# Optimization experiments

Measured on AMD Instinct MI355X. Metric: run time of the kernel, lower is better.

Reference implementation:

```python
import jax, jax.numpy as jnp
import numpy as np
import math

N = 30000        # nodes
E = 390000       # edges (first N are self-loops, in node order)
H = 64
NNS = 4          # num_node_states
NES = 4          # num_edge_states
NGRAPH = 64      # graphs in batch
TEMP_ON_EVAL = 1.0


def from_binary(bits):
    # bits: [..., k] of {0,1} -> integer code sum(bits * 2^k)
    pw = (2 ** jnp.arange(bits.shape[-1])).astype(bits.dtype)
    return jnp.sum(bits * pw, axis=-1)


def segment_softmax(logits, seg, num_seg, tau):
    m = jax.ops.segment_max(logits, seg, num_segments=num_seg)
    e = jnp.exp((logits - m[seg]) / tau)
    s = jax.ops.segment_sum(e, seg, num_segments=num_seg)
    return e / s[seg]


def segment_hard_onehot(logits, seg, num_seg):
    # gumbel_softmax with tau=0, no noise: one-hot at per-segment argmax (first on ties)
    n = logits.shape[0]
    m = jax.ops.segment_max(logits, seg, num_segments=num_seg)
    idx = jnp.where(logits >= m[seg], jnp.arange(n, dtype=jnp.int32), jnp.int32(n))
    first = jax.ops.segment_min(idx, seg, num_segments=num_seg)
    return (jnp.arange(n, dtype=jnp.int32) == first[seg]).astype(jnp.int32)


def select_best(emb, bits, scalars, index, num_index):
    # SelectBest with use_select_best=True. states are even ints < 2^(k+1);
    # unique((states, index)) groups == fused key states*num_index+index.
    states = 2 * from_binary(bits)
    key = states * num_index + index
    num_key = (2 ** (bits.shape[-1] + 1)) * num_index
    best = segment_hard_onehot(-scalars[:, 0], key, num_key)
    return emb[states + best]


def temp_by_step(step, upper, lower, num_iter, temp_on_eval):
    if step == -1:
        return temp_on_eval
    frac = min(float(step) / num_iter, 1.0)
    return upper + (lower - upper) * frac


def forward(node_states, edge_states, scalars, edge_index, batch_vec, rev_idx,
            emb_edge, emb_sbv, emb_sbr, emb_static,
            Wq, Wk, Wv, Wek, Wev, Wc, training_step):
    ei0, ei1 = edge_index[0], edge_index[1]
    # self-loop edges are the first N edges in node order ->
    # scalars[edge_index[0]==edge_index[1]] == scalars[:N]
    node_scalars = scalars[:N]                                   # [N,1]

    # select_best_from_virtual
    node_fts = select_best(emb_sbv, node_states, node_scalars, batch_vec, NGRAPH)  # [N,H]
    edge_fts = emb_edge[from_binary(edge_states)]                # [E,H]

    Q = node_fts @ Wq.T
    K = node_fts @ Wk.T
    V = node_fts @ Wv.T

    # combined_edge_KV
    sb = select_best(emb_sbr, node_states[ei0], scalars, ei1, N)  # [E,H]
    edge_K = sb @ Wek.T
    sender_s = node_scalars[ei0]                                  # [E,1]
    reciever_s = node_scalars[ei1]                                # [E,1]
    rlx = (scalars < reciever_s)
    rlx_d = (sender_s + scalars < reciever_s)
    fts = jnp.concatenate([rlx, rlx_d], axis=-1).astype(jnp.int32)  # [E,2] bits
    static_fts = emb_static[from_binary(fts)]                     # [E,H]
    combined = jnp.concatenate([edge_fts, edge_fts[rev_idx], static_fts], axis=1)  # [E,3H]
    edge_V = combined @ Wc.T                                      # [E,H]

    # compute_message
    Qe = Q[ei1]
    Ke = K[ei0] + edge_K
    Ve = V[ei0] + edge_V
    alpha = jnp.sum(Qe * Ke, axis=-1) / math.sqrt(H)              # [E]
    tau = temp_by_step(int(training_step), 3.0, 0.1, 10000, TEMP_ON_EVAL)
    alpha = segment_softmax(alpha, ei1, N, tau)
    message = Ve * alpha[:, None]                                  # [E,H]

    node_out = node_fts + jax.ops.segment_sum(message, ei1, num_segments=N)
    edge_out = edge_fts + message
    return node_out, edge_out


def setup_inputs() -> dict:
    key = jax.random.key(0)
    ks = jax.random.split(key, 16)
    node_states = jax.random.randint(ks[0], (N, NNS), 0, 2, dtype=jnp.int32)
    edge_states = jax.random.randint(ks[1], (E, NES), 0, 2, dtype=jnp.int32)
    scalars = jax.random.normal(ks[2], (E, 1), dtype=jnp.float32)
    loops = jnp.arange(N, dtype=jnp.int32)
    senders = jax.random.randint(ks[3], (E - N,), 0, N, dtype=jnp.int32)
    receivers = jax.random.randint(ks[4], (E - N,), 0, N, dtype=jnp.int32)
    edge_index = jnp.stack([jnp.concatenate([loops, senders]),
                            jnp.concatenate([loops, receivers])])  # [2,E]
    batch_vec = jnp.sort(jax.random.randint(ks[5], (N,), 0, NGRAPH, dtype=jnp.int32))
    rev_idx = jax.random.permutation(ks[6], E).astype(jnp.int32)
    s = 0.05
    return {
        'node_states': node_states, 'edge_states': edge_states, 'scalars': scalars,
        'edge_index': edge_index, 'batch_vec': batch_vec, 'rev_idx': rev_idx,
        'emb_edge': s * jax.random.normal(ks[7], (2 ** NES, H), dtype=jnp.float32),
        'emb_sbv': s * jax.random.normal(ks[8], (2 ** (NNS + 1), H), dtype=jnp.float32),
        'emb_sbr': s * jax.random.normal(ks[9], (2 ** (NNS + 1), H), dtype=jnp.float32),
        'emb_static': s * jax.random.normal(ks[10], (4, H), dtype=jnp.float32),
        'Wq': s * jax.random.normal(ks[11], (H, H), dtype=jnp.float32),
        'Wk': s * jax.random.normal(ks[12], (H, H), dtype=jnp.float32),
        'Wv': s * jax.random.normal(ks[13], (H, H), dtype=jnp.float32),
        'Wek': s * jax.random.normal(ks[14], (H, H), dtype=jnp.float32),
        'Wev': s * jax.random.normal(ks[15], (H, H), dtype=jnp.float32),
        'Wc': s * jax.random.normal(jax.random.fold_in(key, 99), (H, 3 * H), dtype=jnp.float32),
        'training_step': -1,
    }


def reference(node_states, edge_states, scalars, edge_index, batch_vec, rev_idx,
              emb_edge, emb_sbv, emb_sbr, emb_static,
              Wq, Wk, Wv, Wek, Wev, Wc, training_step):
    return forward(node_states, edge_states, scalars, edge_index, batch_vec, rev_idx,
                   emb_edge, emb_sbv, emb_sbr, emb_static,
                   Wq, Wk, Wv, Wek, Wev, Wc, training_step)
```

## Files before the change

kernel.cpp:

```cpp
#include <hip/hip_runtime.h>

#define NN 30000
#define NE 390000
#define HH 64
#define NGRAPH 64
#define AGG_BLOCKS 1280
#define NE_BLK 1524
#define NN_BLK 118

__device__ __forceinline__ unsigned sortable_f32(float f) {
    unsigned u = __float_as_uint(f);
    return (u & 0x80000000u) ? ~u : (u | 0x80000000u);
}

#define T_V   0
#define T_C1  2048
#define T_C2  3072
#define T_C3  4096
#define T_A   4352
#define T_B   5376
#define T_Q   6400
#define T_K   8448
#define T_EK  10496

__global__ __launch_bounds__(256) void k_init(
        const int4* __restrict__ edge_states, const int4* __restrict__ node_states,
        const float* __restrict__ emb_sbv, const float* __restrict__ emb_sbr,
        const float* __restrict__ emb_edge, const float* __restrict__ emb_static,
        const float* __restrict__ Wq, const float* __restrict__ Wk,
        const float* __restrict__ Wv, const float* __restrict__ Wek,
        const float* __restrict__ Wc,
        unsigned char* __restrict__ esi, int* __restrict__ ns,
        unsigned* __restrict__ cnt, unsigned long long* __restrict__ nodeSel,
        float* __restrict__ tabs) {
    int b = blockIdx.x, t = threadIdx.x;
    if (b < NE_BLK) {
        int e = b * 256 + t;
        if (e < NE) {
            int4 v = edge_states[e];
            esi[e] = (unsigned char)(v.x + 2*v.y + 4*v.z + 8*v.w);
        }
    } else if (b < NE_BLK + NN_BLK) {
        int i = (b - NE_BLK) * 256 + t;
        if (i < NN) {
            int4 v = node_states[i];
            ns[i] = 2 * (v.x + 2*v.y + 4*v.z + 8*v.w);
            cnt[i] = 0u;
        }
    } else if (b < NE_BLK + NN_BLK + 41) {
        int idx = (b - NE_BLK - NN_BLK) * 256 + t;
        if (idx >= 10496) return;
        float acc = 0.f;
        if (idx < 2048) {
            int r = idx >> 6, h = idx & 63;
            for (int j = 0; j < 64; ++j) acc += emb_sbv[r*64+j] * Wv[h*64+j];
            tabs[T_V + idx] = acc;
        } else if (idx < 3072) {
            int x = idx - 2048; int r = x >> 6, h = x & 63;
            for (int j = 0; j < 64; ++j) acc += emb_edge[r*64+j] * Wc[h*192+j];
            tabs[T_C1 + x] = acc;
        } else if (idx < 4096) {
            int x = idx - 3072; int r = x >> 6, h = x & 63;
            for (int j = 0; j < 64; ++j) acc += emb_edge[r*64+j] * Wc[h*192+64+j];
            tabs[T_C2 + x] = acc;
        } else if (idx < 4352) {
            int x = idx - 4096; int r = x >> 6, h = x & 63;
            for (int j = 0; j < 64; ++j) acc += emb_static[r*64+j] * Wc[h*192+128+j];
            tabs[T_C3 + x] = acc;
        } else if (idx < 6400) {
            int x = idx - 4352; int r = x >> 6, h = x & 63;
            for (int j = 0; j < 64; ++j) acc += emb_sbv[r*64+j] * Wq[h*64+j];
            tabs[T_Q + x] = acc;
        } else if (idx < 8448) {
            int x = idx - 6400; int r = x >> 6, h = x & 63;
            for (int j = 0; j < 64; ++j) acc += emb_sbv[r*64+j] * Wk[h*64+j];
            tabs[T_K + x] = acc;
        } else {
            int x = idx - 8448; int r = x >> 6, h = x & 63;
            for (int j = 0; j < 64; ++j) acc += emb_sbr[r*64+j] * Wek[h*64+j];
            tabs[T_EK + x] = acc;
        }
    } else {
        #pragma unroll
        for (int k = 0; k < 4; ++k) nodeSel[t * 4 + k] = ~0ull;
    }
}

__global__ __launch_bounds__(256) void k_phase2(
        const int* __restrict__ ei1, unsigned* __restrict__ cnt,
        unsigned* __restrict__ rank, const int* __restrict__ ns,
        const int* __restrict__ batch_vec, const float* __restrict__ scalars,
        unsigned long long* __restrict__ nodeSel, float* __restrict__ tabs) {
    int b = blockIdx.x, t = threadIdx.x;
    if (b < NE_BLK) {
        int e = b * 256 + t;
        if (e < NE) rank[e] = atomicAdd(&cnt[ei1[e]], 1u);
    } else if (b < NE_BLK + NN_BLK) {
        int i = (b - NE_BLK) * 256 + t;
        if (i < NN) {
            int st = ns[i];
            int key = (st >> 1) * NGRAPH + batch_vec[i];
            unsigned long long pk = ((unsigned long long)sortable_f32(scalars[i]) << 32) | (unsigned)i;
            atomicMin(&nodeSel[key], pk);
        }
    } else {
        int idx = (b - NE_BLK - NN_BLK) * 256 + t;
        if (idx >= 2048) return;
        const float* TQ = tabs + T_Q;
        float acc = 0.f;
        if (idx < 1024) {
            int r1 = idx >> 5, r0 = idx & 31;
            const float* TK = tabs + T_K;
            for (int j = 0; j < 64; ++j) acc += TQ[r1*64+j] * TK[r0*64+j];
            tabs[T_A + idx] = acc * 0.125f;
        } else {
            int x = idx - 1024; int r1 = x >> 5, rk = x & 31;
            const float* TEK = tabs + T_EK;
            for (int j = 0; j < 64; ++j) acc += TQ[r1*64+j] * TEK[rk*64+j];
            tabs[T_B + x] = acc * 0.125f;
        }
    }
}

__global__ __launch_bounds__(256) void k_csr(
        const unsigned* __restrict__ cnt, unsigned* __restrict__ base,
        const int* __restrict__ ns, const int* __restrict__ batch_vec,
        const unsigned long long* __restrict__ nodeSel,
        const float* __restrict__ scalars, uint2* __restrict__ nodePk) {
    int b = blockIdx.x, t = threadIdx.x;
    if (b < NN_BLK) {
        __shared__ unsigned red[256];
        __shared__ unsigned sc[256];
        unsigned pre = 0;
        int lim = b * 256;
        for (int j = t; j < lim; j += 256) pre += cnt[j];
        red[t] = pre;
        __syncthreads();
        for (int o = 128; o > 0; o >>= 1) {
            if (t < o) red[t] += red[t + o];
            __syncthreads();
        }
        unsigned P = red[0];
        int i = lim + t;
        unsigned v = (i < NN) ? cnt[i] : 0u;
        sc[t] = v;
        __syncthreads();
        for (int o = 1; o < 256; o <<= 1) {
            unsigned u = (t >= o) ? sc[t - o] : 0u;
            __syncthreads();
            sc[t] += u;
            __syncthreads();
        }
        if (i < NN) base[i] = P + sc[t] - v;
        if (b == NN_BLK - 1 && t == 255) base[NN] = P + sc[255];
    } else {
        int i = (b - NN_BLK) * 256 + t;
        if (i < NN) {
            int st = ns[i];
            int key = (st >> 1) * NGRAPH + batch_vec[i];
            unsigned win = (unsigned)(nodeSel[key] & 0xffffffffull);
            unsigned row = (unsigned)st + (win == (unsigned)i ? 1u : 0u);
            nodePk[i] = make_uint2(row, __float_as_uint(scalars[i]));
        }
    }
}

__global__ __launch_bounds__(256) void k_edge2(const int* __restrict__ ei0,
        const int* __restrict__ ei1, const uint2* __restrict__ nodePk,
        const unsigned char* __restrict__ esi, const int* __restrict__ rev_idx,
        const float* __restrict__ scalars, const unsigned* __restrict__ base,
        const unsigned* __restrict__ rank, uint2* __restrict__ sKey,
        float* __restrict__ sScal) {
    int e = blockIdx.x * 256 + threadIdx.x;
    if (e >= NE) return;
    int s0 = ei0[e], s1 = ei1[e];
    uint2 np = nodePk[s0];
    unsigned es = esi[e];
    unsigned esr = esi[rev_idx[e]];
    unsigned pos = base[s1] + rank[e];
    sKey[pos] = make_uint2((unsigned)e | (np.x << 19) | (es << 24) | (esr << 28), np.y);
    sScal[pos] = scalars[e];
}

__global__ __launch_bounds__(256) void k_agg(
        const unsigned* __restrict__ base, const uint2* __restrict__ sKey,
        const float* __restrict__ sScal, const uint2* __restrict__ nodePk,
        const float* __restrict__ tabs, const float* __restrict__ emb_edge,
        const float* __restrict__ emb_sbv, const int* __restrict__ step_ptr,
        float* __restrict__ out_node, float* __restrict__ out_edge) {
    __shared__ float lds[7424];
    __shared__ unsigned scr[4][32];
    int tid = threadIdx.x;
    for (int j = tid; j < 6400; j += 256) lds[j] = tabs[j];
    for (int j = tid; j < 1024; j += 256) lds[6400 + j] = emb_edge[j];
    __syncthreads();
    int step = step_ptr[0];
    float invTau;
    if (step == -1) invTau = 1.0f;
    else { float frac = fminf((float)step / 10000.f, 1.f); invTau = 1.0f / (3.0f + (0.1f - 3.0f) * frac); }
    int wid = tid >> 6, lane = tid & 63;
    unsigned* mySc = scr[wid];
    unsigned* myE  = scr[wid] + 16;
    int q = lane >> 4, cidx = (lane & 15) << 2;
    for (int i = blockIdx.x * 4 + wid; i < NN; i += AGG_BLOCKS * 4) {
        unsigned j0 = base[i], j1 = base[i + 1];
        int d = (int)(j1 - j0);
        uint2 np = nodePk[i];
        int r1 = (int)np.x;
        float recv = __uint_as_float(np.y);
        const float* Arow = lds + T_A + r1 * 32;
        const float* Brow = lds + T_B + r1 * 32;
        float4 acc = {0.f, 0.f, 0.f, 0.f};
        if (lane < 16) { mySc[lane] = 0xffffffffu; myE[lane] = 0xffffffffu; }
        __builtin_amdgcn_sched_barrier(0);
        if (d > 0 && d <= 64) {
            bool act = lane < d;
            uint2 key = act ? sKey[j0 + lane] : make_uint2(0u, 0u);
            float sc  = act ? sScal[j0 + lane] : 0.f;
            unsigned scs = sortable_f32(sc);
            unsigned g = (key.x >> 20) & 15u;
            unsigned e19 = key.x & 0x7ffffu;
            if (act) atomicMin(&mySc[g], scs);
            __builtin_amdgcn_sched_barrier(0);
            unsigned ms = mySc[g];
            if (act && scs == ms) atomicMin(&myE[g], e19);
            __builtin_amdgcn_sched_barrier(0);
            bool win = act && (myE[g] == e19);
            int r0 = (key.x >> 19) & 31;
            int ekrow = (r0 & 30) + (win ? 1 : 0);
            float ex = act ? __expf((Arow[r0] + Brow[ekrow]) * invTau) : 0.f;
            float send = __uint_as_float(key.y);
            int si = (sc < recv ? 1 : 0) + (send + sc < recv ? 2 : 0);
            float s = ex;
            #pragma unroll
            for (int o = 1; o < 64; o <<= 1) s += __shfl_xor(s, o);
            float p = ex / s;
            int nIt = (d + 3) >> 2;
            for (int it = 0; it < nIt; ++it) {
                int jj = it * 4 + q;
                unsigned kx = __shfl(key.x, jj);
                int sii = __shfl(si, jj);
                float pp = __shfl(p, jj);
                if (jj < d) {
                    unsigned e = kx & 0x7ffffu;
                    int rr0 = (kx >> 19) & 31, es = (kx >> 24) & 15, esr = (kx >> 28) & 15;
                    float4 tv = *(const float4*)&lds[(rr0 << 6) + cidx];
                    float4 c1 = *(const float4*)&lds[T_C1 + (es << 6) + cidx];
                    float4 c2 = *(const float4*)&lds[T_C2 + (esr << 6) + cidx];
                    float4 c3 = *(const float4*)&lds[T_C3 + (sii << 6) + cidx];
                    float4 ee = *(const float4*)&lds[6400 + (es << 6) + cidx];
                    float4 o;
                    o.x = pp * (tv.x + c1.x + c2.x + c3.x);
                    o.y = pp * (tv.y + c1.y + c2.y + c3.y);
                    o.z = pp * (tv.z + c1.z + c2.z + c3.z);
                    o.w = pp * (tv.w + c1.w + c2.w + c3.w);
                    acc.x += o.x; acc.y += o.y; acc.z += o.z; acc.w += o.w;
                    o.x += ee.x; o.y += ee.y; o.z += ee.z; o.w += ee.w;
                    *(float4*)&out_edge[(size_t)e * 64 + cidx] = o;
                }
            }
        } else if (d > 64) {
            for (unsigned c = j0; c < j1; c += 64) {
                unsigned j = c + lane;
                if (j < j1) {
                    uint2 key = sKey[j];
                    atomicMin(&mySc[(key.x >> 20) & 15u], sortable_f32(sScal[j]));
                }
            }
            __builtin_amdgcn_sched_barrier(0);
            for (unsigned c = j0; c < j1; c += 64) {
                unsigned j = c + lane;
                if (j < j1) {
                    uint2 key = sKey[j];
                    unsigned g = (key.x >> 20) & 15u;
                    if (sortable_f32(sScal[j]) == mySc[g]) atomicMin(&myE[g], key.x & 0x7ffffu);
                }
            }
            __builtin_amdgcn_sched_barrier(0);
            float s = 0.f;
            for (unsigned c = j0; c < j1; c += 64) {
                unsigned j = c + lane;
                if (j < j1) {
                    uint2 key = sKey[j];
                    bool win = (myE[(key.x >> 20) & 15u] == (key.x & 0x7ffffu));
                    int r0 = (key.x >> 19) & 31;
                    int ekrow = (r0 & 30) + (win ? 1 : 0);
                    s += __expf((Arow[r0] + Brow[ekrow]) * invTau);
                }
            }
            #pragma unroll
            for (int o = 1; o < 64; o <<= 1) s += __shfl_xor(s, o);
            float invS = 1.f / s;
            for (unsigned c = j0; c < j1; c += 4) {
                unsigned j = c + q;
                if (j < j1) {
                    uint2 key = sKey[j];
                    float sc = sScal[j];
                    bool win = (myE[(key.x >> 20) & 15u] == (key.x & 0x7ffffu));
                    int r0 = (key.x >> 19) & 31;
                    int ekrow = (r0 & 30) + (win ? 1 : 0);
                    float pp = __expf((Arow[r0] + Brow[ekrow]) * invTau) * invS;
                    float send = __uint_as_float(key.y);
                    int si = (sc < recv ? 1 : 0) + (send + sc < recv ? 2 : 0);
                    unsigned e = key.x & 0x7ffffu;
                    int es = (key.x >> 24) & 15, esr = (key.x >> 28) & 15;
                    float4 tv = *(const float4*)&lds[(r0 << 6) + cidx];
                    float4 c1 = *(const float4*)&lds[T_C1 + (es << 6) + cidx];
                    float4 c2 = *(const float4*)&lds[T_C2 + (esr << 6) + cidx];
                    float4 c3 = *(const float4*)&lds[T_C3 + (si << 6) + cidx];
                    float4 ee = *(const float4*)&lds[6400 + (es << 6) + cidx];
                    float4 o;
                    o.x = pp * (tv.x + c1.x + c2.x + c3.x);
                    o.y = pp * (tv.y + c1.y + c2.y + c3.y);
                    o.z = pp * (tv.z + c1.z + c2.z + c3.z);
                    o.w = pp * (tv.w + c1.w + c2.w + c3.w);
                    acc.x += o.x; acc.y += o.y; acc.z += o.z; acc.w += o.w;
                    o.x += ee.x; o.y += ee.y; o.z += ee.z; o.w += ee.w;
                    *(float4*)&out_edge[(size_t)e * 64 + cidx] = o;
                }
            }
        }
        acc.x += __shfl_xor(acc.x, 16); acc.y += __shfl_xor(acc.y, 16);
        acc.z += __shfl_xor(acc.z, 16); acc.w += __shfl_xor(acc.w, 16);
        acc.x += __shfl_xor(acc.x, 32); acc.y += __shfl_xor(acc.y, 32);
        acc.z += __shfl_xor(acc.z, 32); acc.w += __shfl_xor(acc.w, 32);
        if (lane < 16) {
            float4 nb = *(const float4*)&emb_sbv[(r1 << 6) + cidx];
            float4 o;
            o.x = nb.x + acc.x; o.y = nb.y + acc.y; o.z = nb.z + acc.z; o.w = nb.w + acc.w;
            *(float4*)&out_node[(size_t)i * 64 + cidx] = o;
        }
    }
}

extern "C" void kernel_launch(void* const* d_in, const int* in_sizes, int n_in,
                              void* d_out, int out_size, void* d_ws, size_t ws_size,
                              hipStream_t stream) {
    const int4*  node_states = (const int4*)d_in[0];
    const int4*  edge_states = (const int4*)d_in[1];
    const float* scalars     = (const float*)d_in[2];
    const int*   edge_index  = (const int*)d_in[3];
    const int*   batch_vec   = (const int*)d_in[4];
    const int*   rev_idx     = (const int*)d_in[5];
    const float* emb_edge    = (const float*)d_in[6];
    const float* emb_sbv     = (const float*)d_in[7];
    const float* emb_sbr     = (const float*)d_in[8];
    const float* emb_static  = (const float*)d_in[9];
    const float* Wq  = (const float*)d_in[10];
    const float* Wk  = (const float*)d_in[11];
    const float* Wv  = (const float*)d_in[12];
    const float* Wek = (const float*)d_in[13];
    const float* Wc  = (const float*)d_in[15];
    const int*   step = (const int*)d_in[16];

    const int* ei0 = edge_index;
    const int* ei1 = edge_index + NE;

    char* ws = (char*)d_ws;
    int*      ns     = (int*)(ws);
    uint2*    nodePk = (uint2*)(ws + 120000);
    unsigned char* esi = (unsigned char*)(ws + 360000);
    unsigned* rank   = (unsigned*)(ws + 750016);
    unsigned* cnt    = (unsigned*)(ws + 2310016);
    unsigned* baseA  = (unsigned*)(ws + 2430080);
    uint2*    sKey   = (uint2*)(ws + 2550144);
    float*    sScal  = (float*)(ws + 5670144);
    unsigned long long* nodeSel = (unsigned long long*)(ws + 7230144);
    float*    tabs   = (float*)(ws + 7238336);

    float* out_node = (float*)d_out;
    float* out_edge = out_node + (size_t)NN * HH;

    hipLaunchKernelGGL(k_init, dim3(NE_BLK + NN_BLK + 41 + 1), dim3(256), 0, stream,
                       edge_states, node_states, emb_sbv, emb_sbr, emb_edge, emb_static,
                       Wq, Wk, Wv, Wek, Wc, esi, ns, cnt, nodeSel, tabs);
    hipLaunchKernelGGL(k_phase2, dim3(NE_BLK + NN_BLK + 8), dim3(256), 0, stream,
                       ei1, cnt, rank, ns, batch_vec, scalars, nodeSel, tabs);
    hipLaunchKernelGGL(k_csr, dim3(NN_BLK * 2), dim3(256), 0, stream,
                       cnt, baseA, ns, batch_vec, nodeSel, scalars, nodePk);
    hipLaunchKernelGGL(k_edge2, dim3(NE_BLK), dim3(256), 0, stream,
                       ei0, ei1, nodePk, esi, rev_idx, scalars, baseA, rank, sKey, sScal);
    hipLaunchKernelGGL(k_agg, dim3(AGG_BLOCKS), dim3(256), 0, stream,
                       baseA, sKey, sScal, nodePk, tabs, emb_edge, emb_sbv, step,
                       out_node, out_edge);
}
```

Baseline: 87.72 us.

## Process one node per half-wavefront in aggregation kernel

The aggregation kernel now assigns each node to a 32-lane half-wave instead of a full 64-lane wave, so each block handles 8 nodes and the grid grows to 1875 blocks. Average degree is about 13, so most lanes were idle under the full-wave mapping; halving the group is meant to raise lane utilisation. The high-degree path now loads keys once per 32-chunk and broadcasts them with shuffles, and the node embedding table is staged in LDS. This adds LDS use and more loop iterations per node, and relies on shuffle lane offsets being correct for each half-wave.

```diff
diff --git a/kernel.cpp b/kernel.cpp
--- a/kernel.cpp
+++ b/kernel.cpp
@@ -4,7 +4,7 @@
 #define NE 390000
 #define HH 64
 #define NGRAPH 64
-#define AGG_BLOCKS 1280
+#define AGG_BLOCKS 1875
 #define NE_BLK 1524
 #define NN_BLK 118
 
@@ -188,21 +188,25 @@
         const float* __restrict__ tabs, const float* __restrict__ emb_edge,
         const float* __restrict__ emb_sbv, const int* __restrict__ step_ptr,
         float* __restrict__ out_node, float* __restrict__ out_edge) {
-    __shared__ float lds[7424];
-    __shared__ unsigned scr[4][32];
+    __shared__ float lds[9472];
+    __shared__ unsigned scr[8][33];
     int tid = threadIdx.x;
     for (int j = tid; j < 6400; j += 256) lds[j] = tabs[j];
     for (int j = tid; j < 1024; j += 256) lds[6400 + j] = emb_edge[j];
+    for (int j = tid; j < 2048; j += 256) lds[7424 + j] = emb_sbv[j];
     __syncthreads();
     int step = step_ptr[0];
     float invTau;
     if (step == -1) invTau = 1.0f;
     else { float frac = fminf((float)step / 10000.f, 1.f); invTau = 1.0f / (3.0f + (0.1f - 3.0f) * frac); }
-    int wid = tid >> 6, lane = tid & 63;
-    unsigned* mySc = scr[wid];
-    unsigned* myE  = scr[wid] + 16;
-    int q = lane >> 4, cidx = (lane & 15) << 2;
-    for (int i = blockIdx.x * 4 + wid; i < NN; i += AGG_BLOCKS * 4) {
+    int grp = tid >> 5;
+    int gw  = (tid >> 5) & 1;
+    int l32 = tid & 31;
+    unsigned* mySc = scr[grp];
+    unsigned* myE  = scr[grp] + 16;
+    int sub = l32 >> 4;
+    int cidx = (l32 & 15) << 2;
+    for (int i = blockIdx.x * 8 + grp; i < NN; i += AGG_BLOCKS * 8) {
         unsigned j0 = base[i], j1 = base[i + 1];
         int d = (int)(j1 - j0);
         uint2 np = nodePk[i];
@@ -211,12 +215,12 @@
         const float* Arow = lds + T_A + r1 * 32;
         const float* Brow = lds + T_B + r1 * 32;
         float4 acc = {0.f, 0.f, 0.f, 0.f};
-        if (lane < 16) { mySc[lane] = 0xffffffffu; myE[lane] = 0xffffffffu; }
+        scr[grp][l32] = 0xffffffffu;
         __builtin_amdgcn_sched_barrier(0);
-        if (d > 0 && d <= 64) {
-            bool act = lane < d;
-            uint2 key = act ? sKey[j0 + lane] : make_uint2(0u, 0u);
-            float sc  = act ? sScal[j0 + lane] : 0.f;
+        if (d > 0 && d <= 32) {
+            bool act = l32 < d;
+            uint2 key = act ? sKey[j0 + l32] : make_uint2(0u, 0u);
+            float sc  = act ? sScal[j0 + l32] : 0.f;
             unsigned scs = sortable_f32(sc);
             unsigned g = (key.x >> 20) & 15u;
             unsigned e19 = key.x & 0x7ffffu;
@@ -232,15 +236,17 @@
             float send = __uint_as_float(key.y);
             int si = (sc < recv ? 1 : 0) + (send + sc < recv ? 2 : 0);
             float s = ex;
-            #pragma unroll
-            for (int o = 1; o < 64; o <<= 1) s += __shfl_xor(s, o);
+            s += __shfl_xor(s, 1);  s += __shfl_xor(s, 2);
+            s += __shfl_xor(s, 4);  s += __shfl_xor(s, 8);
+            s += __shfl_xor(s, 16);
             float p = ex / s;
-            int nIt = (d + 3) >> 2;
+            int nIt = (d + 1) >> 1;
             for (int it = 0; it < nIt; ++it) {
-                int jj = it * 4 + q;
-                unsigned kx = __shfl(key.x, jj);
-                int sii = __shfl(si, jj);
-                float pp = __shfl(p, jj);
+                int jj = it * 2 + sub;
+                int sl = (gw << 5) + jj;
+                unsigned kx = __shfl(key.x, sl);
+                int sii = __shfl(si, sl);
+                float pp = __shfl(p, sl);
                 if (jj < d) {
                     unsigned e = kx & 0x7ffffu;
                     int rr0 = (kx >> 19) & 31, es = (kx >> 24) & 15, esr = (kx >> 28) & 15;
@@ -259,17 +265,17 @@
                     *(float4*)&out_edge[(size_t)e * 64 + cidx] = o;
                 }
             }
-        } else if (d > 64) {
-            for (unsigned c = j0; c < j1; c += 64) {
-                unsigned j = c + lane;
+        } else if (d > 32) {
+            for (unsigned c = j0; c < j1; c += 32) {
+                unsigned j = c + l32;
                 if (j < j1) {
                     uint2 key = sKey[j];
                     atomicMin(&mySc[(key.x >> 20) & 15u], sortable_f32(sScal[j]));
                 }
             }
             __builtin_amdgcn_sched_barrier(0);
-            for (unsigned c = j0; c < j1; c += 64) {
-                unsigned j = c + lane;
+            for (unsigned c = j0; c < j1; c += 32) {
+                unsigned j = c + l32;
                 if (j < j1) {
                     uint2 key = sKey[j];
                     unsigned g = (key.x >> 20) & 15u;
@@ -278,8 +284,8 @@
             }
             __builtin_amdgcn_sched_barrier(0);
             float s = 0.f;
-            for (unsigned c = j0; c < j1; c += 64) {
-                unsigned j = c + lane;
+            for (unsigned c = j0; c < j1; c += 32) {
+                unsigned j = c + l32;
                 if (j < j1) {
                     uint2 key = sKey[j];
                     bool win = (myE[(key.x >> 20) & 15u] == (key.x & 0x7ffffu));
@@ -288,44 +294,53 @@
                     s += __expf((Arow[r0] + Brow[ekrow]) * invTau);
                 }
             }
-            #pragma unroll
-            for (int o = 1; o < 64; o <<= 1) s += __shfl_xor(s, o);
+            s += __shfl_xor(s, 1);  s += __shfl_xor(s, 2);
+            s += __shfl_xor(s, 4);  s += __shfl_xor(s, 8);
+            s += __shfl_xor(s, 16);
             float invS = 1.f / s;
-            for (unsigned c = j0; c < j1; c += 4) {
-                unsigned j = c + q;
-                if (j < j1) {
-                    uint2 key = sKey[j];
-                    float sc = sScal[j];
-                    bool win = (myE[(key.x >> 20) & 15u] == (key.x & 0x7ffffu));
-                    int r0 = (key.x >> 19) & 31;
-                    int ekrow = (r0 & 30) + (win ? 1 : 0);
-                    float pp = __expf((Arow[r0] + Brow[ekrow]) * invTau) * invS;
-                    float send = __uint_as_float(key.y);
-                    int si = (sc < recv ? 1 : 0) + (send + sc < recv ? 2 : 0);
-                    unsigned e = key.x & 0x7ffffu;
-                    int es = (key.x >> 24) & 15, esr = (key.x >> 28) & 15;
-                    float4 tv = *(const float4*)&lds[(r0 << 6) + cidx];
-                    float4 c1 = *(const float4*)&lds[T_C1 + (es << 6) + cidx];
-                    float4 c2 = *(const float4*)&lds[T_C2 + (esr << 6) + cidx];
-                    float4 c3 = *(const float4*)&lds[T_C3 + (si << 6) + cidx];
-                    float4 ee = *(const float4*)&lds[6400 + (es << 6) + cidx];
-                    float4 o;
-                    o.x = pp * (tv.x + c1.x + c2.x + c3.x);
-                    o.y = pp * (tv.y + c1.y + c2.y + c3.y);
-                    o.z = pp * (tv.z + c1.z + c2.z + c3.z);
-                    o.w = pp * (tv.w + c1.w + c2.w + c3.w);
-                    acc.x += o.x; acc.y += o.y; acc.z += o.z; acc.w += o.w;
-                    o.x += ee.x; o.y += ee.y; o.z += ee.z; o.w += ee.w;
-                    *(float4*)&out_edge[(size_t)e * 64 + cidx] = o;
+            for (unsigned c = j0; c < j1; c += 32) {
+                int rem = (int)(j1 - c) < 32 ? (int)(j1 - c) : 32;
+                bool act = l32 < rem;
+                uint2 key = act ? sKey[c + l32] : make_uint2(0u, 0u);
+                float sc  = act ? sScal[c + l32] : 0.f;
+                unsigned e19 = key.x & 0x7ffffu;
+                bool win = act && (myE[(key.x >> 20) & 15u] == e19);
+                int r0 = (key.x >> 19) & 31;
+                int ekrow = (r0 & 30) + (win ? 1 : 0);
+                float pp0 = act ? __expf((Arow[r0] + Brow[ekrow]) * invTau) * invS : 0.f;
+                float send = __uint_as_float(key.y);
+                int si = (sc < recv ? 1 : 0) + (send + sc < recv ? 2 : 0);
+                int nIt = (rem + 1) >> 1;
+                for (int it = 0; it < nIt; ++it) {
+                    int jj = it * 2 + sub;
+                    int sl = (gw << 5) + jj;
+                    unsigned kx = __shfl(key.x, sl);
+                    int sii = __shfl(si, sl);
+                    float pp = __shfl(pp0, sl);
+                    if (jj < rem) {
+                        unsigned e = kx & 0x7ffffu;
+                        int rr0 = (kx >> 19) & 31, es = (kx >> 24) & 15, esr = (kx >> 28) & 15;
+                        float4 tv = *(const float4*)&lds[(rr0 << 6) + cidx];
+                        float4 c1 = *(const float4*)&lds[T_C1 + (es << 6) + cidx];
+                        float4 c2 = *(const float4*)&lds[T_C2 + (esr << 6) + cidx];
+                        float4 c3 = *(const float4*)&lds[T_C3 + (sii << 6) + cidx];
+                        float4 ee = *(const float4*)&lds[6400 + (es << 6) + cidx];
+                        float4 o;
+                        o.x = pp * (tv.x + c1.x + c2.x + c3.x);
+                        o.y = pp * (tv.y + c1.y + c2.y + c3.y);
+                        o.z = pp * (tv.z + c1.z + c2.z + c3.z);
+                        o.w = pp * (tv.w + c1.w + c2.w + c3.w);
+                        acc.x += o.x; acc.y += o.y; acc.z += o.z; acc.w += o.w;
+                        o.x += ee.x; o.y += ee.y; o.z += ee.z; o.w += ee.w;
+                        *(float4*)&out_edge[(size_t)e * 64 + cidx] = o;
+                    }
                 }
             }
         }
         acc.x += __shfl_xor(acc.x, 16); acc.y += __shfl_xor(acc.y, 16);
         acc.z += __shfl_xor(acc.z, 16); acc.w += __shfl_xor(acc.w, 16);
-        acc.x += __shfl_xor(acc.x, 32); acc.y += __shfl_xor(acc.y, 32);
-        acc.z += __shfl_xor(acc.z, 32); acc.w += __shfl_xor(acc.w, 32);
-        if (lane < 16) {
-            float4 nb = *(const float4*)&emb_sbv[(r1 << 6) + cidx];
+        if (sub == 0) {
+            float4 nb = *(const float4*)&lds[7424 + (r1 << 6) + cidx];
             float4 o;
             o.x = nb.x + acc.x; o.y = nb.y + acc.y; o.z = nb.z + acc.z; o.w = nb.w + acc.w;
             *(float4*)&out_node[(size_t)i * 64 + cidx] = o;
```

Measured after the change: 91.07 us. 3.8% more time.
